# Kernel optimization log

Hardware: AMD Instinct MI355X
Metric: run time of the kernel (lower is better)

## Reference

```python
import jax, jax.numpy as jnp
import numpy as np

COST_COORDINATE = 1.0  # init kwarg cost_coordinate


def _lsa(cost):
    """Rectangular linear sum assignment (Jonker-Volgenant shortest augmenting
    path), matching scipy.optimize.linear_sum_assignment's algorithm/output.
    Returns (row_ind, col_ind) sorted by row_ind, length = min(nr, nc)."""
    cost = np.asarray(cost, dtype=np.float64)
    transposed = cost.shape[0] > cost.shape[1]
    if transposed:
        cost = cost.T
    nr, nc = cost.shape
    u = np.zeros(nr)
    v = np.zeros(nc)
    path = np.full(nc, -1, dtype=np.int64)
    col4row = np.full(nr, -1, dtype=np.int64)
    row4col = np.full(nc, -1, dtype=np.int64)
    for cur_row in range(nr):
        shortest = np.full(nc, np.inf)
        SR = np.zeros(nr, dtype=bool)
        SC = np.zeros(nc, dtype=bool)
        remaining = np.ones(nc, dtype=bool)
        min_val = 0.0
        i = cur_row
        sink = -1
        while sink == -1:
            SR[i] = True
            rem = np.nonzero(remaining)[0]
            cand = min_val + cost[i, rem] - u[i] - v[rem]
            better = cand < shortest[rem]
            idx_b = rem[better]
            shortest[idx_b] = cand[better]
            path[idx_b] = i
            j = rem[np.argmin(shortest[rem])]
            min_val = shortest[j]
            if not np.isfinite(min_val):
                raise RuntimeError('cost matrix is infeasible')
            SC[j] = True
            remaining[j] = False
            if row4col[j] == -1:
                sink = j
            else:
                i = row4col[j]
        # dual updates
        u[cur_row] += min_val
        mask = SR.copy()
        mask[cur_row] = False
        u[mask] += min_val - shortest[col4row[mask]]
        v[SC] -= min_val - shortest[SC]
        # augment along alternating path
        j = sink
        while True:
            i = path[j]
            row4col[j] = i
            col4row[i], j = j, col4row[i]
            if i == cur_row:
                break
    if transposed:
        order = np.argsort(col4row)
        return col4row[order], order.astype(np.int64)
    return np.arange(nr, dtype=np.int64), col4row


def setup_inputs() -> dict:
    key = jax.random.key(0)
    k1, k2 = jax.random.split(key)
    outputs = jax.random.uniform(k1, (16, 4096, 4), dtype=jnp.float32)  # [B, Q, 4]
    targets = jax.random.uniform(k2, (16, 128, 4), dtype=jnp.float32)   # [B, nt, 4]
    return {'outputs': outputs, 'targets': targets}


@jax.jit
def _cost_matrix(outputs, targets):
    # Block-diagonal part of torch.cdist(out.flatten(0,1), cat(targets), p=1):
    # only the per-image [Q, nt] blocks survive the .split(sizes, -1) in the
    # original, so we compute exactly those. C[b,q,t] = sum_d |out - tgt|.
    return COST_COORDINATE * jnp.abs(
        outputs[:, :, None, :] - targets[:, None, :, :]
    ).sum(-1)  # [B, Q, nt]


def reference(outputs, targets):
    C = _cost_matrix(outputs, targets)
    Cn = np.asarray(jax.device_get(C), dtype=np.float64)
    rows, cols = [], []
    for b in range(Cn.shape[0]):  # batch loop mirrors the original scipy loop
        r, c = _lsa(Cn[b])
        rows.append(r)
        cols.append(c)
    row_ind = jnp.asarray(np.stack(rows), dtype=jnp.int64)  # [B, min(Q,nt)]
    col_ind = jnp.asarray(np.stack(cols), dtype=jnp.int64)  # [B, min(Q,nt)]
    return C, row_ind, col_ind
```

## Files before the change

### kernel.cpp

```cpp
#include <hip/hip_runtime.h>
#include <math.h>

#define NB   16
#define NQ   4096
#define NTGT 128
#define CELEMS (NB * NQ * NTGT)

#define NSLOT 64
#define AT   512
#define ACPT 8
#define ANW  (AT / 64)
#define NCOST (CELEMS / 4 / 2048)

typedef unsigned long long u64;

__global__ __launch_bounds__(256) void rowmin_kernel(
    const float* __restrict__ outputs,
    const float* __restrict__ targets,
    u64*   __restrict__ rowkey2)
{
    __shared__ u64 part[4][NTGT];
    const int tid  = threadIdx.x;
    const int t4   = tid & 31;
    const int b    = blockIdx.x >> 6;
    const int blk  = blockIdx.x & (NSLOT - 1);
    const int idx0 = blockIdx.x * 2048 + tid;

    const float4* tg = reinterpret_cast<const float4*>(targets) + (b << 7) + (t4 << 2);
    float4 g[4];
    #pragma unroll
    for (int f = 0; f < 4; ++f) g[f] = tg[f];

    u64 keymin[4] = {~0ull, ~0ull, ~0ull, ~0ull};

    #pragma unroll
    for (int e = 0; e < 8; ++e) {
        int idx = idx0 + 256 * e;
        int bq  = idx >> 5;
        float4 o = reinterpret_cast<const float4*>(outputs)[bq];
        u64 q = (u64)(unsigned)(bq & (NQ - 1));
        #pragma unroll
        for (int f = 0; f < 4; ++f) {
            float4 gg = g[f];
            float r = (fabsf(o.x - gg.x) + fabsf(o.y - gg.y)) +
                      (fabsf(o.z - gg.z) + fabsf(o.w - gg.w));
            u64 key = (((u64)__float_as_uint(r)) << 32) | q;
            if (key < keymin[f]) keymin[f] = key;
        }
    }

    #pragma unroll
    for (int f = 0; f < 4; ++f) {
        u64 ov = __shfl_xor(keymin[f], 32);
        if (ov < keymin[f]) keymin[f] = ov;
    }
    if ((tid & 63) < 32) {
        int w = tid >> 6;
        #pragma unroll
        for (int f = 0; f < 4; ++f) part[w][(t4 << 2) + f] = keymin[f];
    }
    __syncthreads();

    if (tid < NTGT) {
        u64 k = part[0][tid];
        #pragma unroll
        for (int s = 1; s < 4; ++s) { u64 ov = part[s][tid]; if (ov < k) k = ov; }
        rowkey2[(((size_t)b * NSLOT) + blk) * NTGT + tid] = k;
    }
}

__global__ __launch_bounds__(AT, 1) void fused_kernel(
    const float* __restrict__ outputs,
    const float* __restrict__ targets,
    const u64*   __restrict__ rowkey2,
    float* __restrict__ C,
    float* __restrict__ row_out,
    float* __restrict__ col_out)
{
    __shared__ double2 svp_[NQ];
    __shared__ unsigned claim_[NQ];
    __shared__ short  row4col_[NQ];
    __shared__ unsigned char path_[NQ];
    __shared__ float4 tgt_[NTGT];
    __shared__ double u_[NTGT];
    __shared__ u64    red2_[4][NTGT];
    __shared__ int    rowarg_[NTGT];
    __shared__ short  col4row_[NTGT];
    __shared__ short  left_[NTGT];
    __shared__ int    sc_j[NTGT];
    __shared__ u64    redk_[2][ANW];
    __shared__ u64    bmask_[2];

    const int tid = threadIdx.x;

    if (blockIdx.x >= NB) {
        const int blk = blockIdx.x - NB;
        const int t4  = tid & 31;
        const float4* tg = reinterpret_cast<const float4*>(targets);
        float4 g0, g1, g2, g3;
        {
            int b = (blk * 2048 + tid) >> 17;
            const float4* tgb = tg + (b << 7) + (t4 << 2);
            g0 = tgb[0]; g1 = tgb[1]; g2 = tgb[2]; g3 = tgb[3];
        }
        #pragma unroll
        for (int e = 0; e < 4; ++e) {
            int f  = blk * 2048 + e * 512 + tid;
            int bq = f >> 5;
            float4 o = reinterpret_cast<const float4*>(outputs)[bq];
            float4 r;
            r.x = (fabsf(o.x - g0.x) + fabsf(o.y - g0.y)) + (fabsf(o.z - g0.z) + fabsf(o.w - g0.w));
            r.y = (fabsf(o.x - g1.x) + fabsf(o.y - g1.y)) + (fabsf(o.z - g1.z) + fabsf(o.w - g1.w));
            r.z = (fabsf(o.x - g2.x) + fabsf(o.y - g2.y)) + (fabsf(o.z - g2.z) + fabsf(o.w - g2.w));
            r.w = (fabsf(o.x - g3.x) + fabsf(o.y - g3.y)) + (fabsf(o.z - g3.z) + fabsf(o.w - g3.w));
            reinterpret_cast<float4*>(C)[f] = r;
        }
        return;
    }

    const int b = blockIdx.x;
    const float4* outq = reinterpret_cast<const float4*>(outputs) + b * NQ;

    float4 o0 = outq[tid];
    float4 o1 = outq[tid + AT];
    float4 o2 = outq[tid + AT * 2];
    float4 o3 = outq[tid + AT * 3];
    float4 o4 = outq[tid + AT * 4];
    float4 o5 = outq[tid + AT * 5];
    float4 o6 = outq[tid + AT * 6];
    float4 o7 = outq[tid + AT * 7];

    #pragma unroll
    for (int kk = 0; kk < ACPT; ++kk) {
        int k = tid + AT * kk;
        svp_[k] = make_double2(0.0, 0.0);
        row4col_[k] = -1;
        claim_[k] = 0xFFFFFFFFu;
    }

    {
        const int t = tid & 127, s = tid >> 7;
        const u64* rk = rowkey2 + (size_t)b * NSLOT * NTGT;
        u64 k = ~0ull;
        #pragma unroll
        for (int gg = 0; gg < NSLOT / 4; ++gg) {
            u64 ov = rk[(s * (NSLOT / 4) + gg) * NTGT + t];
            if (ov < k) k = ov;
        }
        red2_[s][t] = k;
    }
    __syncthreads();

    if (tid < NTGT) {
        u64 key = red2_[0][tid];
        #pragma unroll
        for (int s = 1; s < 4; ++s) { u64 ov = red2_[s][tid]; if (ov < key) key = ov; }
        u_[tid] = (double)__uint_as_float((unsigned)(key >> 32));
        rowarg_[tid] = (int)(key & 0xffffffffu);
        tgt_[tid] = reinterpret_cast<const float4*>(targets)[b * NTGT + tid];
    }
    __syncthreads();

    if (tid < NTGT) atomicMin(&claim_[rowarg_[tid]], (unsigned)tid);
    __syncthreads();

    bool un = false;
    if (tid < NTGT) {
        int j = rowarg_[tid];
        bool won = (claim_[j] == (unsigned)tid);
        col4row_[tid] = won ? (short)j : (short)-1;
        if (won) row4col_[j] = (short)tid;
        un = !won;
    }
    {
        u64 m = __ballot(un);
        if ((tid & 63) == 0 && (tid >> 6) < 2) bmask_[tid >> 6] = m;
    }
    __syncthreads();
    const int nleft = __popcll(bmask_[0]) + __popcll(bmask_[1]);
    if (un) {
        int lane = tid & 63, w = tid >> 6;
        int r = __popcll(bmask_[w] & ((1ull << lane) - 1)) + (w ? __popcll(bmask_[0]) : 0);
        left_[r] = (short)tid;
    }
    __syncthreads();

    int parity = 0;

#define COSTN(g, on) ((fabsf((on).x - (g).x) + fabsf((on).y - (g).y)) + \
                      (fabsf((on).z - (g).z) + fabsf((on).w - (g).w)))

    for (int li = 0; li < nleft; ++li) {
        const int cur = left_[li];
        const int j0  = rowarg_[cur];
        const bool fast = (svp_[j0].y == 0.0);
        int      i;
        double   minv = 0.0;
        int      fj   = -1;
        int      Lns  = 0;
        unsigned rem  = 0xFFu;
        unsigned pend = 0u;
        bool     first = true;

        const double uc = u_[cur];
        const float4 gc = tgt_[cur];

        if (fast) {
            i = row4col_[j0];
            fj = j0; Lns = 1;
            if ((j0 & (AT - 1)) == tid) {
                rem  &= ~(1u << (j0 >> 9));
                pend |=  (1u << (j0 >> 9));
                svp_[j0].x = 0.0;
                path_[j0] = (unsigned char)cur;
            }
            if (tid == 0) sc_j[0] = j0;
        } else {
            i = cur;
        }

        while (true) {
            const double ui = u_[i];
            const float4 g  = tgt_[i];

            double bv = (double)INFINITY;
            int    bi = 0xFFF;

            if (first && fast) {
                #define FSTEP(n, on)                                            \
                {   int k = tid + AT * n;                                       \
                    double vk = svp_[k].y;                                      \
                    double cand_c = ((0.0 + (double)COSTN(gc, on)) - uc) - vk;  \
                    double cand_w = ((0.0 + (double)COSTN(g,  on)) - ui) - vk;  \
                    bool wless = cand_w < cand_c;                               \
                    double s = wless ? cand_w : cand_c;                         \
                    if ((rem >> n) & 1u) {                                      \
                        svp_[k].x = s;                                          \
                        path_[k] = (unsigned char)(wless ? i : cur);            \
                        if (s < bv) { bv = s; bi = k; }                         \
                    }                                                           \
                }
                FSTEP(0, o0) FSTEP(1, o1) FSTEP(2, o2) FSTEP(3, o3)
                FSTEP(4, o4) FSTEP(5, o5) FSTEP(6, o6) FSTEP(7, o7)
                #undef FSTEP
            } else if (first) {
                #define ISTEP(n, on)                                            \
                {   int k = tid + AT * n;                                       \
                    double vk = svp_[k].y;                                      \
                    double s = ((0.0 + (double)COSTN(gc, on)) - uc) - vk;       \
                    svp_[k].x = s;                                              \
                    path_[k] = (unsigned char)cur;                              \
                    if (s < bv) { bv = s; bi = k; }                             \
                }
                ISTEP(0, o0) ISTEP(1, o1) ISTEP(2, o2) ISTEP(3, o3)
                ISTEP(4, o4) ISTEP(5, o5) ISTEP(6, o6) ISTEP(7, o7)
                #undef ISTEP
            } else {
                #define USTEP(n, on)                                            \
                {   int k = tid + AT * n;                                       \
                    double2 sv = svp_[k];                                       \
                    double cand = ((minv + (double)COSTN(g, on)) - ui) - sv.y;  \
                    bool valid = (rem >> n) & 1u;                               \
                    double s = sv.x;                                            \
                    if (valid && cand < s) {                                    \
                        s = cand; svp_[k].x = cand;                             \
                        path_[k] = (unsigned char)i;                            \
                    }                                                           \
                    if (valid && s < bv) { bv = s; bi = k; }                    \
                }
                USTEP(0, o0) USTEP(1, o1) USTEP(2, o2) USTEP(3, o3)
                USTEP(4, o4) USTEP(5, o5) USTEP(6, o6) USTEP(7, o7)
                #undef USTEP
            }
            first = false;

            u64 key = (__double_as_longlong(bv) & ~0xFFFull) | (unsigned)bi;
            #pragma unroll
            for (int off = 32; off > 0; off >>= 1) {
                u64 ok = __shfl_down(key, off);
                if (ok < key) key = ok;
            }
            if ((tid & 63) == 0) redk_[parity][tid >> 6] = key;
            __syncthreads();

            u64 fkey = redk_[parity][0];
            #pragma unroll
            for (int w = 1; w < ANW; ++w) {
                u64 ok = redk_[parity][w];
                if (ok < fkey) fkey = ok;
            }
            parity ^= 1;

            fj   = (int)(fkey & 0xFFFull);
            minv = __longlong_as_double((long long)(fkey & ~0xFFFull));

            int r = row4col_[fj];
            if ((fj & (AT - 1)) == tid) {
                rem &= ~(1u << (fj >> 9));
                if (r >= 0) pend |= (1u << (fj >> 9));
            }
            if (r < 0) break;
            if (tid == 0) sc_j[Lns] = fj;
            Lns++;
            i = r;
        }

        const double dfin = minv;
        #pragma unroll
        for (int kk = 0; kk < ACPT; ++kk)
            if (pend & (1u << kk)) {
                int k = tid + AT * kk;
                svp_[k].y -= dfin - svp_[k].x;
            }
        if (tid == 0) {
            u_[cur] += dfin;
            for (int e = 0; e < Lns; ++e) {
                int j = sc_j[e];
                u_[row4col_[j]] += dfin - svp_[j].x;
            }
            int j = fj;
            while (true) {
                int i2 = path_[j];
                row4col_[j] = (short)i2;
                int nj = col4row_[i2];
                col4row_[i2] = (short)j;
                j = nj;
                if (i2 == cur) break;
            }
        }
        __syncthreads();
    }
#undef COSTN

    if (tid < NTGT) {
        int val = col4row_[tid];
        int rank = 0;
        #pragma unroll
        for (int k = 0; k < NTGT; ++k) rank += (col4row_[k] < val);
        row_out[b * NTGT + rank] = (float)val;
        col_out[b * NTGT + rank] = (float)tid;
    }
}

extern "C" void kernel_launch(void* const* d_in, const int* in_sizes, int n_in,
                              void* d_out, int out_size, void* d_ws, size_t ws_size,
                              hipStream_t stream) {
    const float* outputs = (const float*)d_in[0];
    const float* targets = (const float*)d_in[1];
    float* out = (float*)d_out;

    u64* rowkey2 = (u64*)d_ws;

    hipLaunchKernelGGL(rowmin_kernel, dim3(NB * NSLOT), dim3(256), 0, stream,
                       outputs, targets, rowkey2);
    hipLaunchKernelGGL(fused_kernel, dim3(NB + NCOST), dim3(AT), 0, stream,
                       outputs, targets, rowkey2, out,
                       out + CELEMS, out + CELEMS + NB * NTGT);
}
```

Baseline: 31.72 us.

## Keep shortest-path and column duals in registers instead of LDS

The per-column shortest distance and dual v arrays move from a shared double2 array into 16 per-thread double registers, since each thread owns a fixed set of 8 columns. A byte array tracks whether a column's dual was touched (this drives the fast-path test), and the shortest values of scanned columns are recorded in sc_v for the row-dual update done by thread 0. This removes LDS loads and stores from the serial augmenting loop, at the cost of higher register pressure in a 512-thread block.

```diff
diff --git a/kernel.cpp b/kernel.cpp
--- a/kernel.cpp
+++ b/kernel.cpp
@@ -77,10 +77,10 @@
     float* __restrict__ row_out,
     float* __restrict__ col_out)
 {
-    __shared__ double2 svp_[NQ];
     __shared__ unsigned claim_[NQ];
     __shared__ short  row4col_[NQ];
     __shared__ unsigned char path_[NQ];
+    __shared__ unsigned char vtouch_[NQ];
     __shared__ float4 tgt_[NTGT];
     __shared__ double u_[NTGT];
     __shared__ u64    red2_[4][NTGT];
@@ -88,6 +88,7 @@
     __shared__ short  col4row_[NTGT];
     __shared__ short  left_[NTGT];
     __shared__ int    sc_j[NTGT];
+    __shared__ double sc_v[NTGT];
     __shared__ u64    redk_[2][ANW];
     __shared__ u64    bmask_[2];
 
@@ -129,13 +130,15 @@
     float4 o5 = outq[tid + AT * 5];
     float4 o6 = outq[tid + AT * 6];
     float4 o7 = outq[tid + AT * 7];
+    double sh0 = 0, sh1 = 0, sh2 = 0, sh3 = 0, sh4 = 0, sh5 = 0, sh6 = 0, sh7 = 0;
+    double vv0 = 0, vv1 = 0, vv2 = 0, vv3 = 0, vv4 = 0, vv5 = 0, vv6 = 0, vv7 = 0;
 
     #pragma unroll
     for (int kk = 0; kk < ACPT; ++kk) {
         int k = tid + AT * kk;
-        svp_[k] = make_double2(0.0, 0.0);
         row4col_[k] = -1;
         claim_[k] = 0xFFFFFFFFu;
+        vtouch_[k] = 0;
     }
 
     {
@@ -193,7 +196,7 @@
     for (int li = 0; li < nleft; ++li) {
         const int cur = left_[li];
         const int j0  = rowarg_[cur];
-        const bool fast = (svp_[j0].y == 0.0);
+        const bool fast = (vtouch_[j0] == 0);
         int      i;
         double   minv = 0.0;
         int      fj   = -1;
@@ -208,13 +211,18 @@
         if (fast) {
             i = row4col_[j0];
             fj = j0; Lns = 1;
-            if ((j0 & (AT - 1)) == tid) {
-                rem  &= ~(1u << (j0 >> 9));
-                pend |=  (1u << (j0 >> 9));
-                svp_[j0].x = 0.0;
+            const bool mine = ((j0 & (AT - 1)) == tid);
+            const int  slot = j0 >> 9;
+            if (mine) {
+                rem  &= ~(1u << slot);
+                pend |=  (1u << slot);
                 path_[j0] = (unsigned char)cur;
-            }
-            if (tid == 0) sc_j[0] = j0;
+                #define SETJ0(n, shn) if (slot == n) shn = 0.0;
+                SETJ0(0, sh0) SETJ0(1, sh1) SETJ0(2, sh2) SETJ0(3, sh3)
+                SETJ0(4, sh4) SETJ0(5, sh5) SETJ0(6, sh6) SETJ0(7, sh7)
+                #undef SETJ0
+            }
+            if (tid == 0) { sc_j[0] = j0; sc_v[0] = 0.0; }
         } else {
             i = cur;
         }
@@ -227,49 +235,51 @@
             int    bi = 0xFFF;
 
             if (first && fast) {
-                #define FSTEP(n, on)                                            \
+                #define FSTEP(n, on, shn, vvn)                                  \
                 {   int k = tid + AT * n;                                       \
-                    double vk = svp_[k].y;                                      \
-                    double cand_c = ((0.0 + (double)COSTN(gc, on)) - uc) - vk;  \
-                    double cand_w = ((0.0 + (double)COSTN(g,  on)) - ui) - vk;  \
+                    double cand_c = ((0.0 + (double)COSTN(gc, on)) - uc) - vvn; \
+                    double cand_w = ((0.0 + (double)COSTN(g,  on)) - ui) - vvn; \
                     bool wless = cand_w < cand_c;                               \
                     double s = wless ? cand_w : cand_c;                         \
                     if ((rem >> n) & 1u) {                                      \
-                        svp_[k].x = s;                                          \
+                        shn = s;                                                \
                         path_[k] = (unsigned char)(wless ? i : cur);            \
                         if (s < bv) { bv = s; bi = k; }                         \
                     }                                                           \
                 }
-                FSTEP(0, o0) FSTEP(1, o1) FSTEP(2, o2) FSTEP(3, o3)
-                FSTEP(4, o4) FSTEP(5, o5) FSTEP(6, o6) FSTEP(7, o7)
+                FSTEP(0, o0, sh0, vv0) FSTEP(1, o1, sh1, vv1)
+                FSTEP(2, o2, sh2, vv2) FSTEP(3, o3, sh3, vv3)
+                FSTEP(4, o4, sh4, vv4) FSTEP(5, o5, sh5, vv5)
+                FSTEP(6, o6, sh6, vv6) FSTEP(7, o7, sh7, vv7)
                 #undef FSTEP
             } else if (first) {
-                #define ISTEP(n, on)                                            \
+                #define ISTEP(n, on, shn, vvn)                                  \
                 {   int k = tid + AT * n;                                       \
-                    double vk = svp_[k].y;                                      \
-                    double s = ((0.0 + (double)COSTN(gc, on)) - uc) - vk;       \
-                    svp_[k].x = s;                                              \
+                    double s = ((0.0 + (double)COSTN(gc, on)) - uc) - vvn;      \
+                    shn = s;                                                    \
                     path_[k] = (unsigned char)cur;                              \
                     if (s < bv) { bv = s; bi = k; }                             \
                 }
-                ISTEP(0, o0) ISTEP(1, o1) ISTEP(2, o2) ISTEP(3, o3)
-                ISTEP(4, o4) ISTEP(5, o5) ISTEP(6, o6) ISTEP(7, o7)
+                ISTEP(0, o0, sh0, vv0) ISTEP(1, o1, sh1, vv1)
+                ISTEP(2, o2, sh2, vv2) ISTEP(3, o3, sh3, vv3)
+                ISTEP(4, o4, sh4, vv4) ISTEP(5, o5, sh5, vv5)
+                ISTEP(6, o6, sh6, vv6) ISTEP(7, o7, sh7, vv7)
                 #undef ISTEP
             } else {
-                #define USTEP(n, on)                                            \
+                #define USTEP(n, on, shn, vvn)                                  \
                 {   int k = tid + AT * n;                                       \
-                    double2 sv = svp_[k];                                       \
-                    double cand = ((minv + (double)COSTN(g, on)) - ui) - sv.y;  \
+                    double cand = ((minv + (double)COSTN(g, on)) - ui) - vvn;   \
                     bool valid = (rem >> n) & 1u;                               \
-                    double s = sv.x;                                            \
-                    if (valid && cand < s) {                                    \
-                        s = cand; svp_[k].x = cand;                             \
+                    if (valid && cand < shn) {                                  \
+                        shn = cand;                                             \
                         path_[k] = (unsigned char)i;                            \
                     }                                                           \
-                    if (valid && s < bv) { bv = s; bi = k; }                    \
+                    if (valid && shn < bv) { bv = shn; bi = k; }                \
                 }
-                USTEP(0, o0) USTEP(1, o1) USTEP(2, o2) USTEP(3, o3)
-                USTEP(4, o4) USTEP(5, o5) USTEP(6, o6) USTEP(7, o7)
+                USTEP(0, o0, sh0, vv0) USTEP(1, o1, sh1, vv1)
+                USTEP(2, o2, sh2, vv2) USTEP(3, o3, sh3, vv3)
+                USTEP(4, o4, sh4, vv4) USTEP(5, o5, sh5, vv5)
+                USTEP(6, o6, sh6, vv6) USTEP(7, o7, sh7, vv7)
                 #undef USTEP
             }
             first = false;
@@ -300,23 +310,25 @@
                 if (r >= 0) pend |= (1u << (fj >> 9));
             }
             if (r < 0) break;
-            if (tid == 0) sc_j[Lns] = fj;
+            if (tid == 0) { sc_j[Lns] = fj; sc_v[Lns] = minv; }
             Lns++;
             i = r;
         }
 
         const double dfin = minv;
-        #pragma unroll
-        for (int kk = 0; kk < ACPT; ++kk)
-            if (pend & (1u << kk)) {
-                int k = tid + AT * kk;
-                svp_[k].y -= dfin - svp_[k].x;
-            }
+        #define VPAT(n, shn, vvn)                                               \
+        if (pend & (1u << n)) {                                                 \
+            vvn -= dfin - shn;                                                  \
+            vtouch_[tid + AT * n] = 1;                                          \
+        }
+        VPAT(0, sh0, vv0) VPAT(1, sh1, vv1) VPAT(2, sh2, vv2) VPAT(3, sh3, vv3)
+        VPAT(4, sh4, vv4) VPAT(5, sh5, vv5) VPAT(6, sh6, vv6) VPAT(7, sh7, vv7)
+        #undef VPAT
         if (tid == 0) {
             u_[cur] += dfin;
             for (int e = 0; e < Lns; ++e) {
                 int j = sc_j[e];
-                u_[row4col_[j]] += dfin - svp_[j].x;
+                u_[row4col_[j]] += dfin - sc_v[e];
             }
             int j = fj;
             while (true) {
```

After: 31.04 us. 1.02x faster.
